# Optimization experiments

Hardware: AMD Instinct MI355X
Metric: run time of the kernel (lower is better)

## Reference

```python
import jax, jax.numpy as jnp
import numpy as np

N_NODES = 4194304  # 2**22
LEVELS = 10
COARSE = 8192
RANK = 2
NNZ = 8388608


def _interp_linear(u, N):
    """torch F.interpolate(mode='linear', align_corners=False) along axis 1. u: (B,M,R) -> (B,N,R)."""
    M = u.shape[1]
    pos = (jnp.arange(N, dtype=jnp.float32) + 0.5) * (M / N) - 0.5
    pos = jnp.clip(pos, 0.0, M - 1)
    i0 = jnp.floor(pos).astype(jnp.int32)
    i1 = jnp.minimum(i0 + 1, M - 1)
    w = (pos - i0.astype(jnp.float32))[None, :, None]
    return u[:, i0] * (1.0 - w) + u[:, i1] * w


def _apply_hodlr(diag, u_factors, v_factors, x):
    B, N, _ = x.shape
    y = diag * x
    L = u_factors.shape[0]
    for lvl in range(L):
        num_splits = 2 ** (lvl + 1)
        bs = N // num_splits
        if bs == 0:
            continue
        uc, vc = u_factors[lvl], v_factors[lvl]
        u_full = _interp_linear(uc, N) if uc.shape[1] != N else uc
        v_full = _interp_linear(vc, N) if vc.shape[1] != N else vc
        P = num_splits // 2
        valid = P * 2 * bs
        xv = x[:, :valid].reshape(B, P, 2, bs, 1)
        uv = u_full[:, :valid].reshape(B, P, 2, bs, -1)
        vv = v_full[:, :valid].reshape(B, P, 2, bs, -1)
        xL, xR = xv[:, :, 0], xv[:, :, 1]
        uL, uR = uv[:, :, 0], uv[:, :, 1]
        vL, vR = vv[:, :, 0], vv[:, :, 1]
        xRp = jnp.einsum('bpkr,bpko->bpro', vR, xR)  # (B,P,R,1)
        xLp = jnp.einsum('bpkr,bpko->bpro', vL, xL)
        yL = jnp.einsum('bpkr,bpro->bpko', uL, xRp)  # (B,P,bs,1)
        yR = jnp.einsum('bpkr,bpro->bpko', uR, xLp)
        upd = jnp.stack([yL, yR], axis=2).reshape(B, valid, 1)
        if valid < N:
            upd = jnp.pad(upd, ((0, 0), (0, N - valid), (0, 0)))
        y = y + upd
    return y


def setup_inputs() -> dict:
    key = jax.random.key(0)
    ks = jax.random.split(key, 6)
    diag = jax.random.uniform(ks[0], (1, N_NODES, 1), dtype=jnp.float32)
    u_factors = jax.random.normal(ks[1], (LEVELS, 1, COARSE, RANK), dtype=jnp.float32)
    v_factors = jax.random.normal(ks[2], (LEVELS, 1, COARSE, RANK), dtype=jnp.float32)
    A_values = jax.random.normal(ks[3], (NNZ,), dtype=jnp.float32)
    z = jax.random.normal(ks[4], (1, N_NODES, 1), dtype=jnp.float32)
    A_indices = jax.random.randint(ks[5], (2, NNZ), 0, N_NODES, dtype=jnp.int64) if jax.config.jax_enable_x64 else jax.random.randint(ks[5], (2, NNZ), 0, N_NODES, dtype=jnp.int32)
    return {"diag": diag, "u_factors": u_factors, "v_factors": v_factors,
            "A_values": A_values, "z": z, "A_indices": A_indices, "num_nodes": N_NODES}


def reference(diag, u_factors, v_factors, A_values, z, A_indices, num_nodes):
    N = num_nodes
    w = _apply_hodlr(diag, u_factors, v_factors, z)          # (1,N,1)
    w_flat = w.reshape(N)
    rows, cols = A_indices[0], A_indices[1]
    y_flat = jax.ops.segment_sum(A_values * w_flat[cols], rows, num_segments=N)
    y = y_flat.reshape(1, N, 1)
    loss = jnp.mean((y - z) ** 2)
    return loss
```

## Files before the change

kernel.cpp:

```cpp
#include <hip/hip_runtime.h>

#define N_NODES   4194304
#define LEVELS    10
#define COARSE    8192
#define NNZ_E     8388608
#define NCHUNK    16384
#define NBUCK     256
#define BROWS     16384
#define BSH       14
#define HBLOCKS   2048
#define EPB       4096

typedef int          v4i __attribute__((ext_vector_type(4)));
typedef float        v4f __attribute__((ext_vector_type(4)));
typedef unsigned int v4u __attribute__((ext_vector_type(4)));

static __device__ __forceinline__ unsigned short f2bf(float x) {
    unsigned u = __float_as_uint(x);
    return (unsigned short)((u + 0x7FFFu + ((u >> 16) & 1u)) >> 16);
}
static __device__ __forceinline__ float bf2f(unsigned short h) {
    return __uint_as_float((unsigned)h << 16);
}
static __device__ __forceinline__ unsigned pack18(int lrow, float p) {
    unsigned u = __float_as_uint(p);
    return ((unsigned)lrow << 18) | (((u + 0x2000u) >> 14) & 0x3FFFFu);
}

__global__ __launch_bounds__(256) void kA_moments(const float* __restrict__ z,
                                                  float2* __restrict__ M,
                                                  float* __restrict__ S,
                                                  float* __restrict__ out) {
    if (blockIdx.x == 0) {
        for (int i = threadIdx.x; i < 2046 * 2; i += 256) S[i] = 0.f;
        if (threadIdx.x == 0) out[0] = 0.f;
    }
    int lane = threadIdx.x & 63;
    int wave = threadIdx.x >> 6;
    int chunk = blockIdx.x * 4 + wave;
    int base = chunk * 256 + lane * 4;
    float4 zv = *(const float4*)(z + base);
    float a0 = 0.f, a1 = 0.f;
    const float* zp = (const float*)&zv;
#pragma unroll
    for (int j = 0; j < 4; ++j) {
        float p = ((float)(base + j) + 0.5f) * (1.0f / 512.0f) - 0.5f;
        p = fminf(fmaxf(p, 0.0f), (float)(COARSE - 1));
        float f = p - floorf(p);
        a0 += zp[j] * (1.0f - f);
        a1 += zp[j] * f;
    }
#pragma unroll
    for (int off = 32; off >= 1; off >>= 1) {
        a0 += __shfl_xor(a0, off, 64);
        a1 += __shfl_xor(a1, off, 64);
    }
    if (lane == 0) M[chunk] = make_float2(a0, a1);
}

__global__ __launch_bounds__(1024) void kB_ssum(const float2* __restrict__ M,
                                                const float* __restrict__ V,
                                                float* __restrict__ S) {
    int lvl = blockIdx.x >> 3;
    int slice = blockIdx.x & 7;
    int t = threadIdx.x;
    const float2* Vl = (const float2*)(V + lvl * COARSE * 2);
    float s0 = 0.f, s1 = 0.f;
    int c0 = slice * 2048 + t * 2;
#pragma unroll
    for (int cc = 0; cc < 2; ++cc) {
        int c = c0 + cc;
        float2 m = M[c];
        int k = (c > 0) ? ((c - 1) >> 1) : 0;
        int kp = min(k + 1, COARSE - 1);
        float2 vk = Vl[k], vkp = Vl[kp];
        s0 += vk.x * m.x + vkp.x * m.y;
        s1 += vk.y * m.x + vkp.y * m.y;
    }
    int tpg_sh = 12 - lvl;
    int gw = min(1 << tpg_sh, 64);
    for (int sh = gw >> 1; sh >= 1; sh >>= 1) {
        s0 += __shfl_xor(s0, sh, 64);
        s1 += __shfl_xor(s1, sh, 64);
    }
    if ((t & (gw - 1)) == 0) {
        int b = c0 >> (13 - lvl);
        int soff = (2 << lvl) - 2;
        unsafeAtomicAdd(&S[(soff + b) * 2 + 0], s0);
        unsafeAtomicAdd(&S[(soff + b) * 2 + 1], s1);
    }
}

__global__ __launch_bounds__(256) void kC_g(const float* __restrict__ S,
                                            const float* __restrict__ U,
                                            float2* __restrict__ G) {
    int c = blockIdx.x * 256 + threadIdx.x;
    int k = (c > 0) ? ((c - 1) >> 1) : 0;
    int kp = min(k + 1, COARSE - 1);
    float g0 = 0.f, g1 = 0.f;
#pragma unroll
    for (int lvl = 0; lvl < LEVELS; ++lvl) {
        int sib = (c >> (13 - lvl)) ^ 1;
        int soff = (2 << lvl) - 2;
        float2 s = ((const float2*)S)[soff + sib];
        const float2* Ul = (const float2*)(U + lvl * COARSE * 2);
        float2 uk = Ul[k], ukp = Ul[kp];
        g0 += uk.x * s.x + uk.y * s.y;
        g1 += ukp.x * s.x + ukp.y * s.y;
    }
    G[c] = make_float2(g0, g1);
}

__global__ __launch_bounds__(256) void kW(const float* __restrict__ diag,
                                          const float* __restrict__ z,
                                          const float2* __restrict__ G,
                                          unsigned short* __restrict__ wb) {
    int tid = blockIdx.x * 256 + threadIdx.x;
    int base = tid * 4;
    float2 g = G[base >> 8];
    v4f d4 = __builtin_nontemporal_load((const v4f*)(diag + base));
    v4f z4 = __builtin_nontemporal_load((const v4f*)(z + base));
    const float* dp = (const float*)&d4;
    const float* zp = (const float*)&z4;
    ushort4 h4;
    unsigned short* hp = (unsigned short*)&h4;
#pragma unroll
    for (int j = 0; j < 4; ++j) {
        float p = ((float)(base + j) + 0.5f) * (1.0f / 512.0f) - 0.5f;
        p = fminf(fmaxf(p, 0.0f), (float)(COARSE - 1));
        float f = p - floorf(p);
        hp[j] = f2bf(dp[j] * zp[j] + (g.x + f * (g.y - g.x)));
    }
    *(ushort4*)(wb + base) = h4;
}

__global__ __launch_bounds__(256) void kHist(const int* __restrict__ rows,
                                             unsigned int* __restrict__ blockOff) {
    __shared__ unsigned int h[NBUCK];
    int blk = blockIdx.x, t = threadIdx.x;
    h[t] = 0u;
    __syncthreads();
    int base = blk * EPB;
#pragma unroll
    for (int it = 0; it < 4; ++it) {
        int e = base + it * 1024 + t * 4;
        v4i r = __builtin_nontemporal_load((const v4i*)(rows + e));
        atomicAdd(&h[r.x >> BSH], 1u);
        atomicAdd(&h[r.y >> BSH], 1u);
        atomicAdd(&h[r.z >> BSH], 1u);
        atomicAdd(&h[r.w >> BSH], 1u);
    }
    __syncthreads();
    blockOff[t * HBLOCKS + blk] = h[t];
}

__global__ __launch_bounds__(256) void kScan1(unsigned int* __restrict__ blockOff,
                                              unsigned int* __restrict__ total) {
    int b = blockIdx.x, t = threadIdx.x;
    unsigned int* p = blockOff + b * HBLOCKS;
    v4u a = *(const v4u*)(p + t * 8);
    v4u c = *(const v4u*)(p + t * 8 + 4);
    unsigned int s = a.x + a.y + a.z + a.w + c.x + c.y + c.z + c.w;
    unsigned int incl = s;
#pragma unroll
    for (int off = 1; off < 64; off <<= 1) {
        unsigned int n = __shfl_up(incl, off, 64);
        if ((t & 63) >= off) incl += n;
    }
    __shared__ unsigned int wsum[4], wbase[4];
    if ((t & 63) == 63) wsum[t >> 6] = incl;
    __syncthreads();
    if (t == 0) {
        unsigned int acc = 0;
        for (int i = 0; i < 4; ++i) { wbase[i] = acc; acc += wsum[i]; }
        total[b] = acc;
    }
    __syncthreads();
    unsigned int excl = wbase[t >> 6] + incl - s;
    v4u e0, e1;
    e0.x = excl;        e0.y = e0.x + a.x; e0.z = e0.y + a.y; e0.w = e0.z + a.z;
    e1.x = e0.w + a.w;  e1.y = e1.x + c.x; e1.z = e1.y + c.y; e1.w = e1.z + c.z;
    *(v4u*)(p + t * 8) = e0;
    *(v4u*)(p + t * 8 + 4) = e1;
}

__global__ __launch_bounds__(256) void kBinScatter(const int* __restrict__ rows,
                                                   const int* __restrict__ cols,
                                                   const float* __restrict__ vals,
                                                   const unsigned short* __restrict__ wb,
                                                   const unsigned int* __restrict__ blockOff,
                                                   const unsigned int* __restrict__ total,
                                                   unsigned int* __restrict__ packed) {
    __shared__ unsigned int ctr[NBUCK];
    __shared__ unsigned int wsum[4], wbase[4];
    int blk = blockIdx.x, t = threadIdx.x;
    unsigned int tv = total[t];
    unsigned int incl = tv;
#pragma unroll
    for (int off = 1; off < 64; off <<= 1) {
        unsigned int n = __shfl_up(incl, off, 64);
        if ((t & 63) >= off) incl += n;
    }
    if ((t & 63) == 63) wsum[t >> 6] = incl;
    __syncthreads();
    if (t == 0) {
        unsigned int a = 0;
        for (int i = 0; i < 4; ++i) { wbase[i] = a; a += wsum[i]; }
    }
    __syncthreads();
    ctr[t] = (wbase[t >> 6] + incl - tv) + blockOff[t * HBLOCKS + blk];
    __syncthreads();

    int base = blk * EPB;
    v4i r[4], c[4];
    v4f v[4];
#pragma unroll
    for (int j = 0; j < 4; ++j) {
        int e = base + j * 1024 + t * 4;
        r[j] = __builtin_nontemporal_load((const v4i*)(rows + e));
        c[j] = __builtin_nontemporal_load((const v4i*)(cols + e));
        v[j] = __builtin_nontemporal_load((const v4f*)(vals + e));
    }
    unsigned short wv[16];
#pragma unroll
    for (int j = 0; j < 4; ++j) {
        const int* cp = (const int*)&c[j];
        wv[j * 4 + 0] = wb[cp[0]];
        wv[j * 4 + 1] = wb[cp[1]];
        wv[j * 4 + 2] = wb[cp[2]];
        wv[j * 4 + 3] = wb[cp[3]];
    }
#pragma unroll
    for (int j = 0; j < 4; ++j) {
        const int* rp = (const int*)&r[j];
        const float* vp = (const float*)&v[j];
#pragma unroll
        for (int k = 0; k < 4; ++k) {
            int row = rp[k];
            float p = vp[k] * bf2f(wv[j * 4 + k]);
            unsigned int pos = atomicAdd(&ctr[row >> BSH], 1u);
            packed[pos] = pack18(row & (BROWS - 1), p);
        }
    }
}

__global__ __launch_bounds__(1024) void kBucketAccum(const unsigned int* __restrict__ packed,
                                                     const unsigned int* __restrict__ total,
                                                     const float* __restrict__ z,
                                                     float* __restrict__ out) {
    __shared__ float acc[BROWS];
    __shared__ unsigned int sb, sn;
    __shared__ unsigned int wsum[4], wbase[4];
    __shared__ float red[16];
    int b = blockIdx.x, t = threadIdx.x;

    unsigned int tv = 0, incl = 0;
    if (t < 256) {
        tv = total[t];
        incl = tv;
#pragma unroll
        for (int off = 1; off < 64; off <<= 1) {
            unsigned int n = __shfl_up(incl, off, 64);
            if ((t & 63) >= off) incl += n;
        }
        if ((t & 63) == 63) wsum[t >> 6] = incl;
    }
    __syncthreads();
    if (t == 0) {
        unsigned int a = 0;
        for (int i = 0; i < 4; ++i) { wbase[i] = a; a += wsum[i]; }
    }
    __syncthreads();
    if (t < 256 && t == b) { sb = wbase[t >> 6] + incl - tv; sn = tv; }
    for (int i = t; i < BROWS / 4; i += 1024) ((float4*)acc)[i] = make_float4(0.f, 0.f, 0.f, 0.f);
    __syncthreads();

    unsigned int s0 = sb, n = sn;
    for (unsigned int i = t; i < n; i += 1024) {
        unsigned int e = __builtin_nontemporal_load(packed + s0 + i);
        atomicAdd(&acc[e >> 18], __uint_as_float((e & 0x3FFFFu) << 14));
    }
    __syncthreads();

    float part = 0.f;
    int gbase = b * BROWS;
    for (int i = t; i < BROWS; i += 1024) {
        float d = acc[i] - z[gbase + i];
        part += d * d;
    }
#pragma unroll
    for (int off = 32; off >= 1; off >>= 1) part += __shfl_xor(part, off, 64);
    if ((t & 63) == 0) red[t >> 6] = part;
    __syncthreads();
    if (t == 0) {
        float s = 0.f;
        for (int i = 0; i < 16; ++i) s += red[i];
        unsafeAtomicAdd(out, s * (1.0f / (float)N_NODES));
    }
}

extern "C" void kernel_launch(void* const* d_in, const int* in_sizes, int n_in,
                              void* d_out, int out_size, void* d_ws, size_t ws_size,
                              hipStream_t stream) {
    const float* diag  = (const float*)d_in[0];
    const float* U     = (const float*)d_in[1];
    const float* V     = (const float*)d_in[2];
    const float* Avals = (const float*)d_in[3];
    const float* z     = (const float*)d_in[4];
    const int*   Aidx  = (const int*)d_in[5];
    const int* rows = Aidx;
    const int* cols = Aidx + NNZ_E;

    char* ws = (char*)d_ws;
    size_t off = 0;
    unsigned short* wb = (unsigned short*)(ws + off); off += (size_t)N_NODES * 2;
    unsigned int* packed = (unsigned int*)(ws + off); off += (size_t)NNZ_E * 4;
    unsigned int* blockOff = (unsigned int*)(ws + off); off += (size_t)NBUCK * HBLOCKS * 4;
    unsigned int* total    = (unsigned int*)(ws + off); off += NBUCK * 4;
    float2* M  = (float2*)(ws + off); off += NCHUNK * 8;
    float*  S  = (float*)(ws + off);  off += 2046 * 2 * 4;
    float2* G  = (float2*)(ws + off); off += NCHUNK * 8;

    kA_moments<<<NCHUNK / 4, 256, 0, stream>>>(z, M, S, (float*)d_out);
    kB_ssum<<<LEVELS * 8, 1024, 0, stream>>>(M, V, S);
    kC_g<<<NCHUNK / 256, 256, 0, stream>>>(S, U, G);
    kW<<<N_NODES / 1024, 256, 0, stream>>>(diag, z, G, wb);

    kHist<<<HBLOCKS, 256, 0, stream>>>(rows, blockOff);
    kScan1<<<NBUCK, 256, 0, stream>>>(blockOff, total);
    kBinScatter<<<HBLOCKS, 256, 0, stream>>>(rows, cols, Avals, wb, blockOff, total, packed);
    kBucketAccum<<<NBUCK, 1024, 0, stream>>>(packed, total, z, (float*)d_out);
}
```

Measured before the change: 341.6 us.

## Merge independent kernels and locally sort edges before global scatter

The moment kernel and the row histogram now run as one launch, the S-sum and scan share another, and the G computation is folded into the w kernel, cutting the launch count from eight to five. The bin-scatter kernel first sorts each block's 4096 edges by bucket in shared memory, then writes them out in order with nontemporal stores, so global writes become mostly contiguous instead of scattered atomic-indexed stores. In exchange it adds shared-memory traffic and extra barriers, and every w thread now recomputes the per-chunk G sum over all levels.

Measured after the change: 328.0 us. -4.0%, faster.

```diff
diff --git a/kernel.cpp b/kernel.cpp
--- a/kernel.cpp
+++ b/kernel.cpp
@@ -1,15 +1,15 @@
 #include <hip/hip_runtime.h>
 
-#define N_NODES   4194304
-#define LEVELS    10
-#define COARSE    8192
-#define NNZ_E     8388608
-#define NCHUNK    16384
-#define NBUCK     256
-#define BROWS     16384
-#define BSH       14
-#define HBLOCKS   2048
-#define EPB       4096
+#define N_NODES 4194304
+#define LEVELS  10
+#define COARSE  8192
+#define NNZ_E   8388608
+#define NCHUNK  16384
+#define NB      256
+#define BROWS   16384
+#define BSH     14
+#define HB      2048
+#define EPB     4096
 
 typedef int          v4i __attribute__((ext_vector_type(4)));
 typedef float        v4f __attribute__((ext_vector_type(4)));
@@ -22,79 +22,130 @@
 static __device__ __forceinline__ float bf2f(unsigned short h) {
     return __uint_as_float((unsigned)h << 16);
 }
-static __device__ __forceinline__ unsigned pack18(int lrow, float p) {
-    unsigned u = __float_as_uint(p);
-    return ((unsigned)lrow << 18) | (((u + 0x2000u) >> 14) & 0x3FFFFu);
-}
-
-__global__ __launch_bounds__(256) void kA_moments(const float* __restrict__ z,
-                                                  float2* __restrict__ M,
-                                                  float* __restrict__ S,
-                                                  float* __restrict__ out) {
-    if (blockIdx.x == 0) {
-        for (int i = threadIdx.x; i < 2046 * 2; i += 256) S[i] = 0.f;
-        if (threadIdx.x == 0) out[0] = 0.f;
-    }
-    int lane = threadIdx.x & 63;
-    int wave = threadIdx.x >> 6;
-    int chunk = blockIdx.x * 4 + wave;
-    int base = chunk * 256 + lane * 4;
-    float4 zv = *(const float4*)(z + base);
-    float a0 = 0.f, a1 = 0.f;
-    const float* zp = (const float*)&zv;
-#pragma unroll
-    for (int j = 0; j < 4; ++j) {
-        float p = ((float)(base + j) + 0.5f) * (1.0f / 512.0f) - 0.5f;
-        p = fminf(fmaxf(p, 0.0f), (float)(COARSE - 1));
-        float f = p - floorf(p);
-        a0 += zp[j] * (1.0f - f);
-        a1 += zp[j] * f;
-    }
-#pragma unroll
-    for (int off = 32; off >= 1; off >>= 1) {
-        a0 += __shfl_xor(a0, off, 64);
-        a1 += __shfl_xor(a1, off, 64);
-    }
-    if (lane == 0) M[chunk] = make_float2(a0, a1);
-}
-
-__global__ __launch_bounds__(1024) void kB_ssum(const float2* __restrict__ M,
-                                                const float* __restrict__ V,
-                                                float* __restrict__ S) {
-    int lvl = blockIdx.x >> 3;
-    int slice = blockIdx.x & 7;
-    int t = threadIdx.x;
-    const float2* Vl = (const float2*)(V + lvl * COARSE * 2);
-    float s0 = 0.f, s1 = 0.f;
-    int c0 = slice * 2048 + t * 2;
-#pragma unroll
-    for (int cc = 0; cc < 2; ++cc) {
-        int c = c0 + cc;
-        float2 m = M[c];
-        int k = (c > 0) ? ((c - 1) >> 1) : 0;
-        int kp = min(k + 1, COARSE - 1);
-        float2 vk = Vl[k], vkp = Vl[kp];
-        s0 += vk.x * m.x + vkp.x * m.y;
-        s1 += vk.y * m.x + vkp.y * m.y;
-    }
-    int tpg_sh = 12 - lvl;
-    int gw = min(1 << tpg_sh, 64);
-    for (int sh = gw >> 1; sh >= 1; sh >>= 1) {
-        s0 += __shfl_xor(s0, sh, 64);
-        s1 += __shfl_xor(s1, sh, 64);
-    }
-    if ((t & (gw - 1)) == 0) {
-        int b = c0 >> (13 - lvl);
-        int soff = (2 << lvl) - 2;
-        unsafeAtomicAdd(&S[(soff + b) * 2 + 0], s0);
-        unsafeAtomicAdd(&S[(soff + b) * 2 + 1], s1);
-    }
-}
-
-__global__ __launch_bounds__(256) void kC_g(const float* __restrict__ S,
-                                            const float* __restrict__ U,
-                                            float2* __restrict__ G) {
-    int c = blockIdx.x * 256 + threadIdx.x;
+static __device__ __forceinline__ unsigned f18(float p) {
+    return ((__float_as_uint(p) + 0x2000u) >> 14) & 0x3FFFFu;
+}
+
+__global__ __launch_bounds__(256) void kD1(const float* __restrict__ z,
+                                           float2* __restrict__ M,
+                                           float* __restrict__ S,
+                                           float* __restrict__ out,
+                                           const int* __restrict__ rows,
+                                           unsigned* __restrict__ blockOff) {
+    int b = blockIdx.x, t = threadIdx.x;
+    if (b < 4096) {
+        if (b == 0) {
+            for (int i = t; i < 2046 * 2; i += 256) S[i] = 0.f;
+            if (t == 0) out[0] = 0.f;
+        }
+        int lane = t & 63, wave = t >> 6;
+        int chunk = b * 4 + wave;
+        int base = chunk * 256 + lane * 4;
+        float4 zv = *(const float4*)(z + base);
+        float a0 = 0.f, a1 = 0.f;
+        const float* zp = (const float*)&zv;
+#pragma unroll
+        for (int j = 0; j < 4; ++j) {
+            float p = ((float)(base + j) + 0.5f) * (1.0f / 512.0f) - 0.5f;
+            p = fminf(fmaxf(p, 0.0f), (float)(COARSE - 1));
+            float f = p - floorf(p);
+            a0 += zp[j] * (1.0f - f);
+            a1 += zp[j] * f;
+        }
+#pragma unroll
+        for (int off = 32; off >= 1; off >>= 1) {
+            a0 += __shfl_xor(a0, off, 64);
+            a1 += __shfl_xor(a1, off, 64);
+        }
+        if (lane == 0) M[chunk] = make_float2(a0, a1);
+    } else {
+        __shared__ unsigned h[NB];
+        int blk = b - 4096;
+        h[t] = 0u;
+        __syncthreads();
+        int base = blk * EPB;
+#pragma unroll
+        for (int it = 0; it < 4; ++it) {
+            int e = base + it * 1024 + t * 4;
+            v4i r = __builtin_nontemporal_load((const v4i*)(rows + e));
+            atomicAdd(&h[r.x >> BSH], 1u); atomicAdd(&h[r.y >> BSH], 1u);
+            atomicAdd(&h[r.z >> BSH], 1u); atomicAdd(&h[r.w >> BSH], 1u);
+        }
+        __syncthreads();
+        blockOff[t * HB + blk] = h[t];
+    }
+}
+
+__global__ __launch_bounds__(256) void kD2(const float2* __restrict__ M,
+                                           const float* __restrict__ V,
+                                           float* __restrict__ S,
+                                           unsigned* __restrict__ blockOff,
+                                           unsigned* __restrict__ total) {
+    int b = blockIdx.x, t = threadIdx.x;
+    if (b < 80) {
+        int lvl = b >> 3, slice = b & 7;
+        const float2* Vl = (const float2*)(V + lvl * COARSE * 2);
+        float s0 = 0.f, s1 = 0.f;
+        int c0 = slice * 2048 + t * 8;
+#pragma unroll
+        for (int cc = 0; cc < 8; ++cc) {
+            int c = c0 + cc;
+            float2 m = M[c];
+            int k = (c > 0) ? ((c - 1) >> 1) : 0;
+            int kp = min(k + 1, COARSE - 1);
+            float2 vk = Vl[k], vkp = Vl[kp];
+            s0 += vk.x * m.x + vkp.x * m.y;
+            s1 += vk.y * m.x + vkp.y * m.y;
+        }
+        int gw = min(1 << (10 - lvl), 64);
+        for (int sh = gw >> 1; sh >= 1; sh >>= 1) {
+            s0 += __shfl_xor(s0, sh, 64);
+            s1 += __shfl_xor(s1, sh, 64);
+        }
+        if ((t & (gw - 1)) == 0) {
+            int bb = c0 >> (13 - lvl);
+            int soff = (2 << lvl) - 2;
+            unsafeAtomicAdd(&S[(soff + bb) * 2 + 0], s0);
+            unsafeAtomicAdd(&S[(soff + bb) * 2 + 1], s1);
+        }
+    } else {
+        int bb = b - 80;
+        __shared__ unsigned wsum[4], wbase[4];
+        unsigned* p = blockOff + bb * HB;
+        v4u a = *(const v4u*)(p + t * 8);
+        v4u c = *(const v4u*)(p + t * 8 + 4);
+        unsigned s = a.x + a.y + a.z + a.w + c.x + c.y + c.z + c.w;
+        unsigned incl = s;
+#pragma unroll
+        for (int off = 1; off < 64; off <<= 1) {
+            unsigned n = __shfl_up(incl, off, 64);
+            if ((t & 63) >= off) incl += n;
+        }
+        if ((t & 63) == 63) wsum[t >> 6] = incl;
+        __syncthreads();
+        if (t == 0) {
+            unsigned acc = 0;
+            for (int i = 0; i < 4; ++i) { wbase[i] = acc; acc += wsum[i]; }
+            total[bb] = acc;
+        }
+        __syncthreads();
+        unsigned excl = wbase[t >> 6] + incl - s;
+        v4u e0, e1;
+        e0.x = excl;       e0.y = e0.x + a.x; e0.z = e0.y + a.y; e0.w = e0.z + a.z;
+        e1.x = e0.w + a.w; e1.y = e1.x + c.x; e1.z = e1.y + c.y; e1.w = e1.z + c.z;
+        *(v4u*)(p + t * 8) = e0;
+        *(v4u*)(p + t * 8 + 4) = e1;
+    }
+}
+
+__global__ __launch_bounds__(256) void kD3(const float* __restrict__ diag,
+                                           const float* __restrict__ z,
+                                           const float* __restrict__ S,
+                                           const float* __restrict__ U,
+                                           unsigned short* __restrict__ wb) {
+    int tid = blockIdx.x * 256 + threadIdx.x;
+    int base = tid * 4;
+    int c = base >> 8;
     int k = (c > 0) ? ((c - 1) >> 1) : 0;
     int kp = min(k + 1, COARSE - 1);
     float g0 = 0.f, g1 = 0.f;
@@ -102,24 +153,14 @@
     for (int lvl = 0; lvl < LEVELS; ++lvl) {
         int sib = (c >> (13 - lvl)) ^ 1;
         int soff = (2 << lvl) - 2;
-        float2 s = ((const float2*)S)[soff + sib];
+        float2 s2 = ((const float2*)S)[soff + sib];
         const float2* Ul = (const float2*)(U + lvl * COARSE * 2);
         float2 uk = Ul[k], ukp = Ul[kp];
-        g0 += uk.x * s.x + uk.y * s.y;
-        g1 += ukp.x * s.x + ukp.y * s.y;
-    }
-    G[c] = make_float2(g0, g1);
-}
-
-__global__ __launch_bounds__(256) void kW(const float* __restrict__ diag,
-                                          const float* __restrict__ z,
-                                          const float2* __restrict__ G,
-                                          unsigned short* __restrict__ wb) {
-    int tid = blockIdx.x * 256 + threadIdx.x;
-    int base = tid * 4;
-    float2 g = G[base >> 8];
-    v4f d4 = __builtin_nontemporal_load((const v4f*)(diag + base));
-    v4f z4 = __builtin_nontemporal_load((const v4f*)(z + base));
+        g0 += uk.x * s2.x + uk.y * s2.y;
+        g1 += ukp.x * s2.x + ukp.y * s2.y;
+    }
+    float4 d4 = *(const float4*)(diag + base);
+    float4 z4 = *(const float4*)(z + base);
     const float* dp = (const float*)&d4;
     const float* zp = (const float*)&z4;
     ushort4 h4;
@@ -129,87 +170,41 @@
         float p = ((float)(base + j) + 0.5f) * (1.0f / 512.0f) - 0.5f;
         p = fminf(fmaxf(p, 0.0f), (float)(COARSE - 1));
         float f = p - floorf(p);
-        hp[j] = f2bf(dp[j] * zp[j] + (g.x + f * (g.y - g.x)));
+        hp[j] = f2bf(dp[j] * zp[j] + (g0 + f * (g1 - g0)));
     }
     *(ushort4*)(wb + base) = h4;
 }
 
-__global__ __launch_bounds__(256) void kHist(const int* __restrict__ rows,
-                                             unsigned int* __restrict__ blockOff) {
-    __shared__ unsigned int h[NBUCK];
+__global__ __launch_bounds__(256) void kD4(const int* __restrict__ rows,
+                                           const int* __restrict__ cols,
+                                           const float* __restrict__ vals,
+                                           const unsigned short* __restrict__ wb,
+                                           const unsigned* __restrict__ blockOff,
+                                           const unsigned* __restrict__ total,
+                                           unsigned* __restrict__ packed) {
+    __shared__ unsigned cur[NB];
+    __shared__ unsigned gb[NB];
+    __shared__ unsigned wsum[4], wbase[4];
+    __shared__ unsigned sortedP[EPB];
+    __shared__ unsigned char sortedB[EPB];
     int blk = blockIdx.x, t = threadIdx.x;
-    h[t] = 0u;
-    __syncthreads();
-    int base = blk * EPB;
-#pragma unroll
-    for (int it = 0; it < 4; ++it) {
-        int e = base + it * 1024 + t * 4;
-        v4i r = __builtin_nontemporal_load((const v4i*)(rows + e));
-        atomicAdd(&h[r.x >> BSH], 1u);
-        atomicAdd(&h[r.y >> BSH], 1u);
-        atomicAdd(&h[r.z >> BSH], 1u);
-        atomicAdd(&h[r.w >> BSH], 1u);
-    }
-    __syncthreads();
-    blockOff[t * HBLOCKS + blk] = h[t];
-}
-
-__global__ __launch_bounds__(256) void kScan1(unsigned int* __restrict__ blockOff,
-                                              unsigned int* __restrict__ total) {
-    int b = blockIdx.x, t = threadIdx.x;
-    unsigned int* p = blockOff + b * HBLOCKS;
-    v4u a = *(const v4u*)(p + t * 8);
-    v4u c = *(const v4u*)(p + t * 8 + 4);
-    unsigned int s = a.x + a.y + a.z + a.w + c.x + c.y + c.z + c.w;
-    unsigned int incl = s;
+
+    cur[t] = 0u;
+    unsigned tv = total[t];
+    unsigned incl = tv;
 #pragma unroll
     for (int off = 1; off < 64; off <<= 1) {
-        unsigned int n = __shfl_up(incl, off, 64);
+        unsigned n = __shfl_up(incl, off, 64);
         if ((t & 63) >= off) incl += n;
     }
-    __shared__ unsigned int wsum[4], wbase[4];
     if ((t & 63) == 63) wsum[t >> 6] = incl;
     __syncthreads();
     if (t == 0) {
-        unsigned int acc = 0;
-        for (int i = 0; i < 4; ++i) { wbase[i] = acc; acc += wsum[i]; }
-        total[b] = acc;
-    }
-    __syncthreads();
-    unsigned int excl = wbase[t >> 6] + incl - s;
-    v4u e0, e1;
-    e0.x = excl;        e0.y = e0.x + a.x; e0.z = e0.y + a.y; e0.w = e0.z + a.z;
-    e1.x = e0.w + a.w;  e1.y = e1.x + c.x; e1.z = e1.y + c.y; e1.w = e1.z + c.z;
-    *(v4u*)(p + t * 8) = e0;
-    *(v4u*)(p + t * 8 + 4) = e1;
-}
-
-__global__ __launch_bounds__(256) void kBinScatter(const int* __restrict__ rows,
-                                                   const int* __restrict__ cols,
-                                                   const float* __restrict__ vals,
-                                                   const unsigned short* __restrict__ wb,
-                                                   const unsigned int* __restrict__ blockOff,
-                                                   const unsigned int* __restrict__ total,
-                                                   unsigned int* __restrict__ packed) {
-    __shared__ unsigned int ctr[NBUCK];
-    __shared__ unsigned int wsum[4], wbase[4];
-    int blk = blockIdx.x, t = threadIdx.x;
-    unsigned int tv = total[t];
-    unsigned int incl = tv;
-#pragma unroll
-    for (int off = 1; off < 64; off <<= 1) {
-        unsigned int n = __shfl_up(incl, off, 64);
-        if ((t & 63) >= off) incl += n;
-    }
-    if ((t & 63) == 63) wsum[t >> 6] = incl;
-    __syncthreads();
-    if (t == 0) {
-        unsigned int a = 0;
+        unsigned a = 0;
         for (int i = 0; i < 4; ++i) { wbase[i] = a; a += wsum[i]; }
     }
     __syncthreads();
-    ctr[t] = (wbase[t >> 6] + incl - tv) + blockOff[t * HBLOCKS + blk];
-    __syncthreads();
+    unsigned bucketBase = wbase[t >> 6] + incl - tv;
 
     int base = blk * EPB;
     v4i r[4], c[4];
@@ -233,41 +228,78 @@
 #pragma unroll
     for (int j = 0; j < 4; ++j) {
         const int* rp = (const int*)&r[j];
+        atomicAdd(&cur[rp[0] >> BSH], 1u);
+        atomicAdd(&cur[rp[1] >> BSH], 1u);
+        atomicAdd(&cur[rp[2] >> BSH], 1u);
+        atomicAdd(&cur[rp[3] >> BSH], 1u);
+    }
+    __syncthreads();
+    unsigned lv = cur[t];
+    unsigned lincl = lv;
+#pragma unroll
+    for (int off = 1; off < 64; off <<= 1) {
+        unsigned n = __shfl_up(lincl, off, 64);
+        if ((t & 63) >= off) lincl += n;
+    }
+    if ((t & 63) == 63) wsum[t >> 6] = lincl;
+    __syncthreads();
+    if (t == 0) {
+        unsigned a = 0;
+        for (int i = 0; i < 4; ++i) { wbase[i] = a; a += wsum[i]; }
+    }
+    __syncthreads();
+    unsigned lexcl = wbase[t >> 6] + lincl - lv;
+    gb[t] = bucketBase + blockOff[t * HB + blk] - lexcl;
+    __syncthreads();
+    cur[t] = lexcl;
+    __syncthreads();
+#pragma unroll
+    for (int j = 0; j < 4; ++j) {
+        const int* rp = (const int*)&r[j];
         const float* vp = (const float*)&v[j];
 #pragma unroll
-        for (int k = 0; k < 4; ++k) {
-            int row = rp[k];
-            float p = vp[k] * bf2f(wv[j * 4 + k]);
-            unsigned int pos = atomicAdd(&ctr[row >> BSH], 1u);
-            packed[pos] = pack18(row & (BROWS - 1), p);
-        }
-    }
-}
-
-__global__ __launch_bounds__(1024) void kBucketAccum(const unsigned int* __restrict__ packed,
-                                                     const unsigned int* __restrict__ total,
-                                                     const float* __restrict__ z,
-                                                     float* __restrict__ out) {
+        for (int kk = 0; kk < 4; ++kk) {
+            int row = rp[kk];
+            unsigned bkt = (unsigned)row >> BSH;
+            float p = vp[kk] * bf2f(wv[j * 4 + kk]);
+            unsigned i = atomicAdd(&cur[bkt], 1u);
+            sortedP[i] = ((unsigned)(row & (BROWS - 1)) << 18) | f18(p);
+            sortedB[i] = (unsigned char)bkt;
+        }
+    }
+    __syncthreads();
+#pragma unroll
+    for (int k = 0; k < 16; ++k) {
+        int i = k * 256 + t;
+        unsigned bkt = sortedB[i];
+        __builtin_nontemporal_store(sortedP[i], packed + gb[bkt] + i);
+    }
+}
+
+__global__ __launch_bounds__(1024) void kD5(const unsigned* __restrict__ packed,
+                                            const unsigned* __restrict__ total,
+                                            const float* __restrict__ z,
+                                            float* __restrict__ out) {
     __shared__ float acc[BROWS];
-    __shared__ unsigned int sb, sn;
-    __shared__ unsigned int wsum[4], wbase[4];
+    __shared__ unsigned sb, sn;
+    __shared__ unsigned wsum[4], wbase[4];
     __shared__ float red[16];
     int b = blockIdx.x, t = threadIdx.x;
 
-    unsigned int tv = 0, incl = 0;
+    unsigned tv = 0, incl = 0;
     if (t < 256) {
         tv = total[t];
         incl = tv;
 #pragma unroll
         for (int off = 1; off < 64; off <<= 1) {
-            unsigned int n = __shfl_up(incl, off, 64);
+            unsigned n = __shfl_up(incl, off, 64);
             if ((t & 63) >= off) incl += n;
         }
         if ((t & 63) == 63) wsum[t >> 6] = incl;
     }
     __syncthreads();
     if (t == 0) {
-        unsigned int a = 0;
+        unsigned a = 0;
         for (int i = 0; i < 4; ++i) { wbase[i] = a; a += wsum[i]; }
     }
     __syncthreads();
@@ -275,9 +307,9 @@
     for (int i = t; i < BROWS / 4; i += 1024) ((float4*)acc)[i] = make_float4(0.f, 0.f, 0.f, 0.f);
     __syncthreads();
 
-    unsigned int s0 = sb, n = sn;
-    for (unsigned int i = t; i < n; i += 1024) {
-        unsigned int e = __builtin_nontemporal_load(packed + s0 + i);
+    unsigned s0 = sb, n = sn;
+    for (unsigned i = t; i < n; i += 1024) {
+        unsigned e = __builtin_nontemporal_load(packed + s0 + i);
         atomicAdd(&acc[e >> 18], __uint_as_float((e & 0x3FFFFu) << 14));
     }
     __syncthreads();
@@ -314,20 +346,15 @@
     char* ws = (char*)d_ws;
     size_t off = 0;
     unsigned short* wb = (unsigned short*)(ws + off); off += (size_t)N_NODES * 2;
-    unsigned int* packed = (unsigned int*)(ws + off); off += (size_t)NNZ_E * 4;
-    unsigned int* blockOff = (unsigned int*)(ws + off); off += (size_t)NBUCK * HBLOCKS * 4;
-    unsigned int* total    = (unsigned int*)(ws + off); off += NBUCK * 4;
-    float2* M  = (float2*)(ws + off); off += NCHUNK * 8;
-    float*  S  = (float*)(ws + off);  off += 2046 * 2 * 4;
-    float2* G  = (float2*)(ws + off); off += NCHUNK * 8;
-
-    kA_moments<<<NCHUNK / 4, 256, 0, stream>>>(z, M, S, (float*)d_out);
-    kB_ssum<<<LEVELS * 8, 1024, 0, stream>>>(M, V, S);
-    kC_g<<<NCHUNK / 256, 256, 0, stream>>>(S, U, G);
-    kW<<<N_NODES / 1024, 256, 0, stream>>>(diag, z, G, wb);
-
-    kHist<<<HBLOCKS, 256, 0, stream>>>(rows, blockOff);
-    kScan1<<<NBUCK, 256, 0, stream>>>(blockOff, total);
-    kBinScatter<<<HBLOCKS, 256, 0, stream>>>(rows, cols, Avals, wb, blockOff, total, packed);
-    kBucketAccum<<<NBUCK, 1024, 0, stream>>>(packed, total, z, (float*)d_out);
-}
+    unsigned* packed   = (unsigned*)(ws + off);       off += (size_t)NNZ_E * 4;
+    unsigned* blockOff = (unsigned*)(ws + off);       off += (size_t)NB * HB * 4;
+    unsigned* total    = (unsigned*)(ws + off);       off += 1024;
+    float2* M          = (float2*)(ws + off);         off += (size_t)NCHUNK * 8;
+    float* S           = (float*)(ws + off);          off += 16384;
+
+    kD1<<<6144, 256, 0, stream>>>(z, M, S, (float*)d_out, rows, blockOff);
+    kD2<<<336, 256, 0, stream>>>(M, V, S, blockOff, total);
+    kD3<<<4096, 256, 0, stream>>>(diag, z, S, U, wb);
+    kD4<<<HB, 256, 0, stream>>>(rows, cols, Avals, wb, blockOff, total, packed);
+    kD5<<<NB, 1024, 0, stream>>>(packed, total, z, (float*)d_out);
+}
```
